# Optimization experiments

Measured on AMD Instinct MI355X. Metric: run time of the kernel, lower is better.

The kernel has to match this reference:

```python
import jax, jax.numpy as jnp
import numpy as np

B, NUM_FRAMES, NUM_PATCHES = 2, 16, 196
DIM, H, DH = 768, 12, 64
T = NUM_FRAMES * NUM_PATCHES  # 3136
EPS = 1e-5


def setup_inputs() -> dict:
    key = jax.random.key(0)
    ks = jax.random.split(key, 5)
    x = jax.random.normal(ks[0], (B, T, DIM), jnp.float32)
    context = jax.random.normal(ks[1], (B, T, DIM), jnp.float32)
    Wq = jax.random.normal(ks[2], (DIM, H * DH), jnp.float32) * 0.02
    Wkv = jax.random.normal(ks[3], (DIM, 2 * H * DH), jnp.float32) * 0.02
    Wo = jax.random.normal(ks[4], (H * DH, DIM), jnp.float32) * 0.02
    bo = jnp.zeros((DIM,), jnp.float32)
    gamma = jnp.ones((DIM,), jnp.float32)
    beta = jnp.zeros((DIM,), jnp.float32)
    # block-diagonal frame mask: patch i attends to patch j iff same frame
    frame_ids = jnp.arange(T) // NUM_PATCHES
    mask = frame_ids[:, None] == frame_ids[None, :]  # [T, T] bool
    return {"x": x, "context": context, "Wq": Wq, "Wkv": Wkv, "Wo": Wo,
            "bo": bo, "gamma": gamma, "beta": beta, "mask": mask}


def reference(x, context, Wq, Wkv, Wo, bo, gamma, beta, mask):
    # LayerNorm on queries only (torch LN: biased variance, eps=1e-5)
    mu = jnp.mean(x, axis=-1, keepdims=True)
    var = jnp.var(x, axis=-1, keepdims=True)
    xn = (x - mu) * jax.lax.rsqrt(var + EPS) * gamma + beta

    q = xn @ Wq                      # [B, T, H*DH]
    kv = context @ Wkv               # [B, T, 2*H*DH]
    k, v = jnp.split(kv, 2, axis=-1)

    def split_heads(t):
        return t.reshape(B, T, H, DH).transpose(0, 2, 1, 3)  # [B, H, T, DH]

    q, k, v = split_heads(q), split_heads(k), split_heads(v)

    scale = DH ** -0.5
    dots = jnp.einsum('bhnd,bhmd->bhnm', q, k) * scale      # [B, H, T, T]
    dots = jnp.where(mask, dots, -jnp.inf)
    attn = jax.nn.softmax(dots, axis=-1)                    # dropout p=0.0 -> identity
    out = jnp.einsum('bhnm,bhmd->bhnd', attn, v)            # [B, H, T, DH]
    out = out.transpose(0, 2, 1, 3).reshape(B, T, H * DH)
    return out @ Wo + bo
```

## Files before the change

kernel.cpp:

```cpp
#include <hip/hip_runtime.h>
#include <hip/hip_bf16.h>

#define NB 2
#define TT 3136
#define DIM 768
#define NH 12
#define NF 16
#define NP 196

typedef __attribute__((ext_vector_type(8))) short short8;
typedef __attribute__((ext_vector_type(4))) short s16x4;
typedef __attribute__((ext_vector_type(4))) float f32x4;
typedef unsigned int uint;

__device__ __forceinline__ float bf2f(short s) {
    return __uint_as_float(((uint)(unsigned short)s) << 16);
}
__device__ __forceinline__ short f2bs(float f) {
    __hip_bfloat16 h = __float2bfloat16(f);
    short s; __builtin_memcpy(&s, &h, 2); return s;
}
__device__ __forceinline__ void load16_lds(const void* g, void* l) {
    __builtin_amdgcn_global_load_lds(
        (const __attribute__((address_space(1))) unsigned int*)g,
        (__attribute__((address_space(3))) unsigned int*)l, 16, 0, 0);
}

__global__ __launch_bounds__(256)
void prep_w(const float* __restrict__ Wq, const float* __restrict__ Wkv,
            const float* __restrict__ Wo,
            __hip_bfloat16* __restrict__ WqT, __hip_bfloat16* __restrict__ WkvT,
            __hip_bfloat16* __restrict__ WoT) {
    __shared__ float tile[32][33];
    int bx = blockIdx.x;
    const float* W; __hip_bfloat16* WT; int N, n0;
    if (bx < 24)      { W = Wq;  WT = WqT;  N = DIM;     n0 = bx * 32; }
    else if (bx < 72) { W = Wkv; WT = WkvT; N = 2 * DIM; n0 = (bx - 24) * 32; }
    else              { W = Wo;  WT = WoT;  N = DIM;     n0 = (bx - 72) * 32; }
    int k0 = blockIdx.y * 32;
    int tx = threadIdx.x & 31, ty = threadIdx.x >> 5;
#pragma unroll
    for (int i = 0; i < 32; i += 8)
        tile[ty + i][tx] = W[(size_t)(k0 + ty + i) * N + (n0 + tx)];
    __syncthreads();
#pragma unroll
    for (int i = 0; i < 32; i += 8)
        WT[(size_t)(n0 + ty + i) * DIM + (k0 + tx)] = __float2bfloat16(tile[tx][ty + i]);
}

__global__ __launch_bounds__(256)
void prep_xc(const float* __restrict__ ctx, __hip_bfloat16* __restrict__ cb,
             const float* __restrict__ x, const float* __restrict__ gamma,
             const float* __restrict__ beta, __hip_bfloat16* __restrict__ xn) {
    int blk = blockIdx.x, tid = threadIdx.x;
    if (blk < 4704) {
        size_t i = (size_t)blk * 256 + tid;
        f32x4 f; __builtin_memcpy(&f, ctx + i * 4, 16);
        s16x4 s;
#pragma unroll
        for (int j = 0; j < 4; j++) s[j] = f2bs(f[j]);
        __builtin_memcpy((short*)cb + i * 4, &s, 8);
        return;
    }
    int row = blk - 4704;
    const float* xr = x + (size_t)row * DIM;
    float v[3], s = 0.f, ss = 0.f;
#pragma unroll
    for (int i = 0; i < 3; i++) {
        v[i] = xr[tid + i * 256];
        s += v[i]; ss += v[i] * v[i];
    }
#pragma unroll
    for (int off = 32; off; off >>= 1) {
        s += __shfl_xor(s, off);
        ss += __shfl_xor(ss, off);
    }
    __shared__ float red[8];
    int wid = tid >> 6, lane = tid & 63;
    if (lane == 0) { red[wid] = s; red[wid + 4] = ss; }
    __syncthreads();
    if (tid == 0) {
        float S = red[0] + red[1] + red[2] + red[3];
        float SS = red[4] + red[5] + red[6] + red[7];
        float mu = S / DIM;
        float var = SS / DIM - mu * mu;
        red[0] = mu;
        red[1] = rsqrtf(var + 1e-5f);
    }
    __syncthreads();
    float mu = red[0], rs = red[1];
#pragma unroll
    for (int i = 0; i < 3; i++) {
        int c = tid + i * 256;
        xn[(size_t)row * DIM + c] = __float2bfloat16((v[i] - mu) * rs * gamma[c] + beta[c]);
    }
}

__global__ __launch_bounds__(256)
void gemm_qkv(const __hip_bfloat16* __restrict__ xn,
              const __hip_bfloat16* __restrict__ cb,
              const __hip_bfloat16* __restrict__ WqT,
              const __hip_bfloat16* __restrict__ WkvT,
              __hip_bfloat16* __restrict__ qbuf,
              __hip_bfloat16* __restrict__ kvbuf) {
    __shared__ short sA[128 * 64];
    __shared__ short sB[128 * 64];
    int y = blockIdx.y;
    const __hip_bfloat16 *A, *BT;
    __hip_bfloat16* C;
    int N, n0;
    if (y < 6) { A = xn; BT = WqT;  C = qbuf;  N = DIM;     n0 = y * 128; }
    else       { A = cb; BT = WkvT; C = kvbuf; N = 2 * DIM; n0 = (y - 6) * 128; }
    int m0 = blockIdx.x * 128;
    int tid = threadIdx.x, lane = tid & 63, wave = tid >> 6;
    int r = lane & 15, q = lane >> 4;
    int wm = (wave & 1) * 64, wn = (wave >> 1) * 64;
    f32x4 acc[4][4] = {};
    for (int k0 = 0; k0 < DIM; k0 += 64) {
#pragma unroll
        for (int i = 0; i < 4; i++) {
            int c = i * 256 + tid;
            int row = c >> 3, cg = c & 7;
            load16_lds(A + (size_t)(m0 + row) * DIM + k0 + cg * 8, &sA[c * 8]);
        }
#pragma unroll
        for (int i = 0; i < 4; i++) {
            int c = i * 256 + tid;
            int row = c >> 3, cg = c & 7;
            load16_lds(BT + (size_t)(n0 + row) * DIM + k0 + cg * 8, &sB[c * 8]);
        }
        __syncthreads();
#pragma unroll
        for (int ks = 0; ks < 2; ks++) {
            short8 af[4], bf[4];
#pragma unroll
            for (int t = 0; t < 4; t++) {
                __builtin_memcpy(&af[t], &sA[(wm + t * 16 + r) * 64 + ks * 32 + q * 8], 16);
                __builtin_memcpy(&bf[t], &sB[(wn + t * 16 + r) * 64 + ks * 32 + q * 8], 16);
            }
#pragma unroll
            for (int mi = 0; mi < 4; mi++)
#pragma unroll
                for (int ni = 0; ni < 4; ni++)
                    acc[mi][ni] = __builtin_amdgcn_mfma_f32_16x16x32_bf16(
                        af[mi], bf[ni], acc[mi][ni], 0, 0, 0);
        }
        __syncthreads();
    }
#pragma unroll
    for (int mi = 0; mi < 4; mi++)
#pragma unroll
        for (int ni = 0; ni < 4; ni++)
#pragma unroll
            for (int rr = 0; rr < 4; rr++) {
                int row = m0 + wm + mi * 16 + q * 4 + rr;
                int col = n0 + wn + ni * 16 + r;
                C[(size_t)row * N + col] = __float2bfloat16(acc[mi][ni][rr]);
            }
}

__global__ __launch_bounds__(256)
void gemm_o(const __hip_bfloat16* __restrict__ A,
            const __hip_bfloat16* __restrict__ BT,
            const float* __restrict__ bias,
            float* __restrict__ C) {
    __shared__ short sA[128 * 64];
    __shared__ short sB[128 * 64];
    int m0 = blockIdx.x * 128, n0 = blockIdx.y * 128;
    int tid = threadIdx.x, lane = tid & 63, wave = tid >> 6;
    int r = lane & 15, q = lane >> 4;
    int wm = (wave & 1) * 64, wn = (wave >> 1) * 64;
    f32x4 acc[4][4] = {};
    for (int k0 = 0; k0 < DIM; k0 += 64) {
#pragma unroll
        for (int i = 0; i < 4; i++) {
            int c = i * 256 + tid;
            int row = c >> 3, cg = c & 7;
            load16_lds(A + (size_t)(m0 + row) * DIM + k0 + cg * 8, &sA[c * 8]);
        }
#pragma unroll
        for (int i = 0; i < 4; i++) {
            int c = i * 256 + tid;
            int row = c >> 3, cg = c & 7;
            load16_lds(BT + (size_t)(n0 + row) * DIM + k0 + cg * 8, &sB[c * 8]);
        }
        __syncthreads();
#pragma unroll
        for (int ks = 0; ks < 2; ks++) {
            short8 af[4], bf[4];
#pragma unroll
            for (int t = 0; t < 4; t++) {
                __builtin_memcpy(&af[t], &sA[(wm + t * 16 + r) * 64 + ks * 32 + q * 8], 16);
                __builtin_memcpy(&bf[t], &sB[(wn + t * 16 + r) * 64 + ks * 32 + q * 8], 16);
            }
#pragma unroll
            for (int mi = 0; mi < 4; mi++)
#pragma unroll
                for (int ni = 0; ni < 4; ni++)
                    acc[mi][ni] = __builtin_amdgcn_mfma_f32_16x16x32_bf16(
                        af[mi], bf[ni], acc[mi][ni], 0, 0, 0);
        }
        __syncthreads();
    }
    float bv[4];
#pragma unroll
    for (int ni = 0; ni < 4; ni++) bv[ni] = bias[n0 + wn + ni * 16 + r];
#pragma unroll
    for (int mi = 0; mi < 4; mi++)
#pragma unroll
        for (int ni = 0; ni < 4; ni++)
#pragma unroll
            for (int rr = 0; rr < 4; rr++) {
                int row = m0 + wm + mi * 16 + q * 4 + rr;
                int col = n0 + wn + ni * 16 + r;
                C[(size_t)row * DIM + col] = acc[mi][ni][rr] + bv[ni];
            }
}

__global__ __launch_bounds__(512)
void attn_kernel(__hip_bfloat16* qo,
                 const __hip_bfloat16* __restrict__ kvb) {
    __shared__ short sQ[64 * 66];
    __shared__ short sKV[14464];
    __shared__ short sP[64 * 226];
    int blk = blockIdx.x;
    int quad = blk & 3;
    int rest = blk >> 2;
    int f = rest % NF, h = (rest / NF) % NH, b = rest / (NF * NH);
    size_t tok0 = (size_t)b * TT + (size_t)f * NP;
    int row0 = quad * 49;
    int tid = threadIdx.x, wave = tid >> 6, lane = tid & 63;
    int r = lane & 15, q = lane >> 4;

    {
        int row = tid >> 3, cg = tid & 7;
        short8 tq = {0,0,0,0,0,0,0,0};
        if (row < 49)
            __builtin_memcpy(&tq, qo + (tok0 + row0 + row) * DIM + h * 64 + cg * 8, 16);
        __builtin_memcpy(&sQ[row * 66 + cg * 8], &tq, 16);
    }
    for (int e = tid; e < 1664; e += 512) {
        int row = e >> 3, cg = e & 7;
        short8 tk = {0,0,0,0,0,0,0,0};
        if (row < NP)
            __builtin_memcpy(&tk, kvb + (tok0 + row) * 1536 + h * 64 + cg * 8, 16);
        __builtin_memcpy(&sKV[row * 66 + cg * 8], &tk, 16);
    }
    __syncthreads();

    for (int t = wave; t < 52; t += 8) {
        int mt = t & 3, nt = t >> 2;
        f32x4 acc = {};
        short8 af, bfv;
        __builtin_memcpy(&af,  &sQ[(mt * 16 + r) * 66 + q * 8], 16);
        __builtin_memcpy(&bfv, &sKV[(nt * 16 + r) * 66 + q * 8], 16);
        acc = __builtin_amdgcn_mfma_f32_16x16x32_bf16(af, bfv, acc, 0, 0, 0);
        __builtin_memcpy(&af,  &sQ[(mt * 16 + r) * 66 + 32 + q * 8], 16);
        __builtin_memcpy(&bfv, &sKV[(nt * 16 + r) * 66 + 32 + q * 8], 16);
        acc = __builtin_amdgcn_mfma_f32_16x16x32_bf16(af, bfv, acc, 0, 0, 0);
#pragma unroll
        for (int rr = 0; rr < 4; rr++)
            sP[(mt * 16 + q * 4 + rr) * 226 + nt * 16 + r] = f2bs(acc[rr] * 0.125f);
    }
    __syncthreads();

    for (int k = 0; k < 8; k++) {
        int row = wave + 8 * k;
        float v[4], m = -INFINITY;
#pragma unroll
        for (int jj = 0; jj < 4; jj++) {
            int c = lane + jj * 64;
            v[jj] = (c < NP) ? bf2f(sP[row * 226 + c]) : -INFINITY;
            m = fmaxf(m, v[jj]);
        }
#pragma unroll
        for (int off = 32; off; off >>= 1) m = fmaxf(m, __shfl_xor(m, off));
        float ps = 0.f;
#pragma unroll
        for (int jj = 0; jj < 4; jj++) {
            int c = lane + jj * 64;
            if (c < NP) { v[jj] = __expf(v[jj] - m); ps += v[jj]; }
        }
#pragma unroll
        for (int off = 32; off; off >>= 1) ps += __shfl_xor(ps, off);
        float inv = 1.f / ps;
#pragma unroll
        for (int jj = 0; jj < 4; jj++) {
            int c = lane + jj * 64;
            if (c < NP)       sP[row * 226 + c] = f2bs(v[jj] * inv);
            else if (c < 224) sP[row * 226 + c] = 0;
        }
    }
    for (int jj = 0; jj < 224; jj += 32) {
        int j = jj + (tid >> 4);
        int d = (tid & 15) * 4;
        s16x4 v = {0, 0, 0, 0};
        if (j < NP)
            __builtin_memcpy(&v, kvb + (tok0 + j) * 1536 + DIM + h * 64 + d, 8);
#pragma unroll
        for (int i = 0; i < 4; i++) sKV[(d + i) * 226 + j] = v[i];
    }
    __syncthreads();

    for (int t = wave; t < 16; t += 8) {
        int mt = t & 3, nt = t >> 2;
        f32x4 acc = {};
#pragma unroll
        for (int kc = 0; kc < 7; kc++) {
            short8 af, bfv;
            __builtin_memcpy(&af,  &sP[(mt * 16 + r) * 226 + kc * 32 + q * 8], 16);
            __builtin_memcpy(&bfv, &sKV[(nt * 16 + r) * 226 + kc * 32 + q * 8], 16);
            acc = __builtin_amdgcn_mfma_f32_16x16x32_bf16(af, bfv, acc, 0, 0, 0);
        }
#pragma unroll
        for (int rr = 0; rr < 4; rr++) {
            int row = mt * 16 + q * 4 + rr;
            if (row < 49)
                qo[(tok0 + row0 + row) * DIM + h * 64 + nt * 16 + r] =
                    __float2bfloat16(acc[rr]);
        }
    }
}

extern "C" void kernel_launch(void* const* d_in, const int* in_sizes, int n_in,
                              void* d_out, int out_size, void* d_ws, size_t ws_size,
                              hipStream_t stream) {
    const float* x     = (const float*)d_in[0];
    const float* ctx   = (const float*)d_in[1];
    const float* Wq    = (const float*)d_in[2];
    const float* Wkv   = (const float*)d_in[3];
    const float* Wo    = (const float*)d_in[4];
    const float* bo    = (const float*)d_in[5];
    const float* gamma = (const float*)d_in[6];
    const float* beta  = (const float*)d_in[7];

    char* ws = (char*)d_ws;
    __hip_bfloat16* cbuf  = (__hip_bfloat16*)(ws + 0);
    __hip_bfloat16* kvbuf = (__hip_bfloat16*)(ws + 9633792);
    __hip_bfloat16* qbuf  = (__hip_bfloat16*)(ws + 28901376);
    __hip_bfloat16* WqT   = (__hip_bfloat16*)(ws + 38535168);
    __hip_bfloat16* WkvT  = (__hip_bfloat16*)(ws + 39714816);
    __hip_bfloat16* WoT   = (__hip_bfloat16*)(ws + 42074112);
    __hip_bfloat16* xnbuf = (__hip_bfloat16*)d_out;
    float*          out   = (float*)d_out;

    prep_w<<<dim3(96, 24), 256, 0, stream>>>(Wq, Wkv, Wo, WqT, WkvT, WoT);
    prep_xc<<<10976, 256, 0, stream>>>(ctx, cbuf, x, gamma, beta, xnbuf);
    gemm_qkv<<<dim3(49, 18), 256, 0, stream>>>(xnbuf, cbuf, WqT, WkvT, qbuf, kvbuf);
    attn_kernel<<<NB * NH * NF * 4, 512, 0, stream>>>(qbuf, kvbuf);
    gemm_o<<<dim3(49, 6), 256, 0, stream>>>(qbuf, WoT, bo, out);
}
```

Baseline: 242.7 us.

## Keep attention scores in registers, softmax per wave, halve attention blocks

Restructures the attention kernel so each wave owns 16 query rows. It computes S^T via MFMA into registers, does the softmax in registers with cross-lane shuffles, and rearranges P into A-operand fragments with shuffles instead of staging it through LDS. Blocks now cover 98 query rows (2 per frame-head) with 448 threads, so K/V are loaded and transposed half as often. This removes the sP LDS round trip and two barriers, at the cost of higher register pressure and fewer, larger blocks.

```diff
diff --git a/kernel.cpp b/kernel.cpp
--- a/kernel.cpp
+++ b/kernel.cpp
@@ -217,107 +217,117 @@
             }
 }
 
-__global__ __launch_bounds__(512)
+__global__ __launch_bounds__(448)
 void attn_kernel(__hip_bfloat16* qo,
                  const __hip_bfloat16* __restrict__ kvb) {
-    __shared__ short sQ[64 * 66];
-    __shared__ short sKV[14464];
-    __shared__ short sP[64 * 226];
+    __shared__ short sQ[112 * 66];
+    __shared__ short sK[208 * 66];
+    __shared__ short sVT[64 * 226];
     int blk = blockIdx.x;
-    int quad = blk & 3;
-    int rest = blk >> 2;
+    int half = blk & 1;
+    int rest = blk >> 1;
     int f = rest % NF, h = (rest / NF) % NH, b = rest / (NF * NH);
     size_t tok0 = (size_t)b * TT + (size_t)f * NP;
-    int row0 = quad * 49;
+    int row0 = half * 98;
     int tid = threadIdx.x, wave = tid >> 6, lane = tid & 63;
     int r = lane & 15, q = lane >> 4;
 
-    {
-        int row = tid >> 3, cg = tid & 7;
-        short8 tq = {0,0,0,0,0,0,0,0};
-        if (row < 49)
-            __builtin_memcpy(&tq, qo + (tok0 + row0 + row) * DIM + h * 64 + cg * 8, 16);
-        __builtin_memcpy(&sQ[row * 66 + cg * 8], &tq, 16);
-    }
-    for (int e = tid; e < 1664; e += 512) {
+    for (int e = tid; e < 896; e += 448) {
         int row = e >> 3, cg = e & 7;
-        short8 tk = {0,0,0,0,0,0,0,0};
+        short8 t = {0,0,0,0,0,0,0,0};
+        if (row < 98)
+            __builtin_memcpy(&t, qo + (tok0 + row0 + row) * DIM + h * 64 + cg * 8, 16);
+        __builtin_memcpy(&sQ[row * 66 + cg * 8], &t, 16);
+    }
+    for (int e = tid; e < 1664; e += 448) {
+        int row = e >> 3, cg = e & 7;
+        short8 t = {0,0,0,0,0,0,0,0};
         if (row < NP)
-            __builtin_memcpy(&tk, kvb + (tok0 + row) * 1536 + h * 64 + cg * 8, 16);
-        __builtin_memcpy(&sKV[row * 66 + cg * 8], &tk, 16);
-    }
-    __syncthreads();
-
-    for (int t = wave; t < 52; t += 8) {
-        int mt = t & 3, nt = t >> 2;
-        f32x4 acc = {};
-        short8 af, bfv;
-        __builtin_memcpy(&af,  &sQ[(mt * 16 + r) * 66 + q * 8], 16);
-        __builtin_memcpy(&bfv, &sKV[(nt * 16 + r) * 66 + q * 8], 16);
-        acc = __builtin_amdgcn_mfma_f32_16x16x32_bf16(af, bfv, acc, 0, 0, 0);
-        __builtin_memcpy(&af,  &sQ[(mt * 16 + r) * 66 + 32 + q * 8], 16);
-        __builtin_memcpy(&bfv, &sKV[(nt * 16 + r) * 66 + 32 + q * 8], 16);
-        acc = __builtin_amdgcn_mfma_f32_16x16x32_bf16(af, bfv, acc, 0, 0, 0);
-#pragma unroll
-        for (int rr = 0; rr < 4; rr++)
-            sP[(mt * 16 + q * 4 + rr) * 226 + nt * 16 + r] = f2bs(acc[rr] * 0.125f);
-    }
-    __syncthreads();
-
-    for (int k = 0; k < 8; k++) {
-        int row = wave + 8 * k;
-        float v[4], m = -INFINITY;
-#pragma unroll
-        for (int jj = 0; jj < 4; jj++) {
-            int c = lane + jj * 64;
-            v[jj] = (c < NP) ? bf2f(sP[row * 226 + c]) : -INFINITY;
-            m = fmaxf(m, v[jj]);
-        }
-#pragma unroll
-        for (int off = 32; off; off >>= 1) m = fmaxf(m, __shfl_xor(m, off));
-        float ps = 0.f;
-#pragma unroll
-        for (int jj = 0; jj < 4; jj++) {
-            int c = lane + jj * 64;
-            if (c < NP) { v[jj] = __expf(v[jj] - m); ps += v[jj]; }
-        }
-#pragma unroll
-        for (int off = 32; off; off >>= 1) ps += __shfl_xor(ps, off);
-        float inv = 1.f / ps;
-#pragma unroll
-        for (int jj = 0; jj < 4; jj++) {
-            int c = lane + jj * 64;
-            if (c < NP)       sP[row * 226 + c] = f2bs(v[jj] * inv);
-            else if (c < 224) sP[row * 226 + c] = 0;
-        }
-    }
-    for (int jj = 0; jj < 224; jj += 32) {
+            __builtin_memcpy(&t, kvb + (tok0 + row) * 1536 + h * 64 + cg * 8, 16);
+        __builtin_memcpy(&sK[row * 66 + cg * 8], &t, 16);
+    }
+    for (int jj = 0; jj < 224; jj += 28) {
         int j = jj + (tid >> 4);
         int d = (tid & 15) * 4;
         s16x4 v = {0, 0, 0, 0};
         if (j < NP)
             __builtin_memcpy(&v, kvb + (tok0 + j) * 1536 + DIM + h * 64 + d, 8);
 #pragma unroll
-        for (int i = 0; i < 4; i++) sKV[(d + i) * 226 + j] = v[i];
+        for (int i = 0; i < 4; i++) sVT[(d + i) * 226 + j] = v[i];
     }
     __syncthreads();
 
-    for (int t = wave; t < 16; t += 8) {
-        int mt = t & 3, nt = t >> 2;
-        f32x4 acc = {};
+    f32x4 sacc[13];
+    short8 qf0, qf1;
+    __builtin_memcpy(&qf0, &sQ[(wave * 16 + r) * 66 + q * 8], 16);
+    __builtin_memcpy(&qf1, &sQ[(wave * 16 + r) * 66 + 32 + q * 8], 16);
+#pragma unroll
+    for (int jf = 0; jf < 13; jf++) {
+        f32x4 a = {};
+        short8 kf;
+        __builtin_memcpy(&kf, &sK[(jf * 16 + r) * 66 + q * 8], 16);
+        a = __builtin_amdgcn_mfma_f32_16x16x32_bf16(kf, qf0, a, 0, 0, 0);
+        __builtin_memcpy(&kf, &sK[(jf * 16 + r) * 66 + 32 + q * 8], 16);
+        a = __builtin_amdgcn_mfma_f32_16x16x32_bf16(kf, qf1, a, 0, 0, 0);
+        sacc[jf] = a;
+    }
+
+    const float scale = 0.125f;
+    float mx = -INFINITY;
+#pragma unroll
+    for (int jf = 0; jf < 13; jf++)
+#pragma unroll
+        for (int rg = 0; rg < 4; rg++) {
+            bool valid = (jf < 12) | (q == 0);
+            if (valid) mx = fmaxf(mx, sacc[jf][rg] * scale);
+        }
+    mx = fmaxf(mx, __shfl_xor(mx, 16));
+    mx = fmaxf(mx, __shfl_xor(mx, 32));
+    float ps = 0.f;
+#pragma unroll
+    for (int jf = 0; jf < 13; jf++)
+#pragma unroll
+        for (int rg = 0; rg < 4; rg++) {
+            bool valid = (jf < 12) | (q == 0);
+            float p = valid ? __expf(sacc[jf][rg] * scale - mx) : 0.f;
+            sacc[jf][rg] = p;
+            ps += p;
+        }
+    ps += __shfl_xor(ps, 16);
+    ps += __shfl_xor(ps, 32);
+    float inv = 1.f / ps;
+
+    int srcl[8];
+#pragma unroll
+    for (int e = 0; e < 8; e++)
+        srcl[e] = ((((q * 8 + e) >> 2) & 3) << 4) | r;
+    short8 pa[7];
+#pragma unroll
+    for (int c = 0; c < 7; c++) {
+#pragma unroll
+        for (int e = 0; e < 8; e++) {
+            float v0 = __shfl(sacc[2 * c][e & 3], srcl[e], 64);
+            float v1 = (c < 6) ? __shfl(sacc[2 * c + 1][e & 3], srcl[e], 64) : 0.f;
+            float val = (q >= 2) ? v1 : v0;
+            pa[c][e] = f2bs(val * inv);
+        }
+    }
+
+#pragma unroll
+    for (int nt = 0; nt < 4; nt++) {
+        f32x4 oacc = {};
 #pragma unroll
         for (int kc = 0; kc < 7; kc++) {
-            short8 af, bfv;
-            __builtin_memcpy(&af,  &sP[(mt * 16 + r) * 226 + kc * 32 + q * 8], 16);
-            __builtin_memcpy(&bfv, &sKV[(nt * 16 + r) * 226 + kc * 32 + q * 8], 16);
-            acc = __builtin_amdgcn_mfma_f32_16x16x32_bf16(af, bfv, acc, 0, 0, 0);
-        }
-#pragma unroll
-        for (int rr = 0; rr < 4; rr++) {
-            int row = mt * 16 + q * 4 + rr;
-            if (row < 49)
-                qo[(tok0 + row0 + row) * DIM + h * 64 + nt * 16 + r] =
-                    __float2bfloat16(acc[rr]);
+            short8 bfv;
+            __builtin_memcpy(&bfv, &sVT[(nt * 16 + r) * 226 + kc * 32 + q * 8], 16);
+            oacc = __builtin_amdgcn_mfma_f32_16x16x32_bf16(pa[kc], bfv, oacc, 0, 0, 0);
+        }
+#pragma unroll
+        for (int rg = 0; rg < 4; rg++) {
+            int local = wave * 16 + q * 4 + rg;
+            if (local < 98)
+                qo[(tok0 + row0 + local) * DIM + h * 64 + nt * 16 + r] =
+                    __float2bfloat16(oacc[rg]);
         }
     }
 }
@@ -347,6 +357,6 @@
     prep_w<<<dim3(96, 24), 256, 0, stream>>>(Wq, Wkv, Wo, WqT, WkvT, WoT);
     prep_xc<<<10976, 256, 0, stream>>>(ctx, cbuf, x, gamma, beta, xnbuf);
     gemm_qkv<<<dim3(49, 18), 256, 0, stream>>>(xnbuf, cbuf, WqT, WkvT, qbuf, kvbuf);
-    attn_kernel<<<NB * NH * NF * 4, 512, 0, stream>>>(qbuf, kvbuf);
+    attn_kernel<<<NB * NH * NF * 2, 448, 0, stream>>>(qbuf, kvbuf);
     gemm_o<<<dim3(49, 6), 256, 0, stream>>>(qbuf, WoT, bo, out);
 }
```

Measured after the change: 219.6 us. -9.5%, faster.
